# Optimization experiments

Hardware: AMD Instinct MI355X
Metric: run time of the kernel (lower is better)

## Reference

```python
import jax, jax.numpy as jnp
import numpy as np

N_NODES = 50000
N_EDGES = 800000
IN_DIM = 512
OUT_DIM = 512


def setup_inputs() -> dict:
    key = jax.random.key(0)
    ks = jax.random.split(key, 8)
    x = jax.random.normal(ks[0], (N_NODES, IN_DIM), dtype=jnp.float32)
    edge_index = jax.random.randint(ks[1], (2, N_EDGES), 0, N_NODES, dtype=jnp.int64)
    s = 1.0 / np.sqrt(IN_DIM)
    # SAGEConv params: lin_l (applied to aggregated neighbors, with bias),
    # lin_r (applied to root/self features, no bias). Two convs: loc and scale.
    Wl1 = jax.random.uniform(ks[2], (OUT_DIM, IN_DIM), jnp.float32, -s, s)
    bl1 = jnp.zeros((OUT_DIM,), jnp.float32)
    Wr1 = jax.random.uniform(ks[3], (OUT_DIM, IN_DIM), jnp.float32, -s, s)
    Wl2 = jax.random.uniform(ks[4], (OUT_DIM, IN_DIM), jnp.float32, -s, s)
    bl2 = jnp.zeros((OUT_DIM,), jnp.float32)
    Wr2 = jax.random.uniform(ks[5], (OUT_DIM, IN_DIM), jnp.float32, -s, s)
    return {"x": x, "edge_index": edge_index,
            "Wl1": Wl1, "bl1": bl1, "Wr1": Wr1,
            "Wl2": Wl2, "bl2": bl2, "Wr2": Wr2}


def _sage_conv(x, agg, Wl, bl, Wr):
    # lin_l(sum-aggregated neighbors) + lin_r(x)
    return agg @ Wl.T + bl + x @ Wr.T


def reference(x, edge_index, Wl1, bl1, Wr1, Wl2, bl2, Wr2):
    src, dst = edge_index[0], edge_index[1]
    # sum aggregation of source features into destination nodes: [N, in_dim]
    agg = jax.ops.segment_sum(x[src], dst, num_segments=N_NODES)
    loc = _sage_conv(x, agg, Wl1, bl1, Wr1)
    loc = jnp.clip(loc, -100.0, 100.0)
    scale = jax.nn.softplus(_sage_conv(x, agg, Wl2, bl2, Wr2)) + 0.001
    scale = jnp.minimum(scale, 100.0)
    return (loc, scale)
```

## Files before the change

kernel.cpp:

```cpp
#include <hip/hip_runtime.h>
#include <stdint.h>

#define N_NODES 50000
#define N_EDGES 800000
#define IN_DIM 512
#define OUT_DIM 512
#define KDIM 1024
#define NDIM 1024

typedef __bf16 bf16x8 __attribute__((ext_vector_type(8)));
typedef float f32x4 __attribute__((ext_vector_type(4)));

__device__ __forceinline__ unsigned short f2bf(float f) {
    union { float f; unsigned u; } c; c.f = f;
    unsigned u = c.u;
    u += 0x7fffu + ((u >> 16) & 1u);
    return (unsigned short)(u >> 16);
}
__device__ __forceinline__ float bf2f(unsigned short h) {
    union { unsigned u; float f; } c; c.u = ((unsigned)h) << 16;
    return c.f;
}

__global__ void xconv_kernel(const float* __restrict__ x, unsigned short* __restrict__ xb) {
    int i = blockIdx.x * blockDim.x + threadIdx.x;
    const int n4 = N_NODES * IN_DIM / 4;
    if (i < n4) {
        float4 v = ((const float4*)x)[i];
        ushort4 o;
        o.x = f2bf(v.x); o.y = f2bf(v.y); o.z = f2bf(v.z); o.w = f2bf(v.w);
        ((ushort4*)xb)[i] = o;
    }
}

__global__ void count_kernel(const int* __restrict__ ei, int* __restrict__ counts) {
    int i = blockIdx.x * blockDim.x + threadIdx.x;
    if (i < N_EDGES) {
        int dst = ei[N_EDGES + i];
        dst = min(max(dst, 0), N_NODES - 1);
        atomicAdd(&counts[dst], 1);
    }
}

__global__ __launch_bounds__(1024) void scan_local_kernel(
    const int* __restrict__ cnt, int* __restrict__ offs,
    int* __restrict__ bsums, int n) {
    __shared__ int warp_sums[16];
    int tid = threadIdx.x;
    int lane = tid & 63;
    int w = tid >> 6;
    int i = blockIdx.x * 1024 + tid;
    int v = (i < n) ? cnt[i] : 0;
    int s = v;
    #pragma unroll
    for (int d = 1; d < 64; d <<= 1) {
        int t = __shfl_up(s, d, 64);
        if (lane >= d) s += t;
    }
    if (lane == 63) warp_sums[w] = s;
    __syncthreads();
    if (w == 0) {
        int ws = (lane < 16) ? warp_sums[lane] : 0;
        #pragma unroll
        for (int d = 1; d < 16; d <<= 1) {
            int t = __shfl_up(ws, d, 64);
            if (lane >= d) ws += t;
        }
        if (lane < 16) warp_sums[lane] = ws;
    }
    __syncthreads();
    int base = (w > 0 ? warp_sums[w - 1] : 0);
    if (i < n) offs[i] = base + s - v;
    if (tid == 1023) bsums[blockIdx.x] = base + s;
}

__global__ void scan_bsums_kernel(int* __restrict__ bsums, int nb) {
    int lane = threadIdx.x & 63;
    int v = (lane < nb) ? bsums[lane] : 0;
    int s = v;
    #pragma unroll
    for (int d = 1; d < 64; d <<= 1) {
        int t = __shfl_up(s, d, 64);
        if (lane >= d) s += t;
    }
    if (lane < nb) bsums[lane] = s - v;
}

__global__ __launch_bounds__(1024) void scan_apply_kernel(
    int* __restrict__ offs, int* __restrict__ cursor,
    const int* __restrict__ bsums, const int* __restrict__ cnt, int n) {
    int i = blockIdx.x * 1024 + threadIdx.x;
    if (i < n) {
        int o = offs[i] + bsums[blockIdx.x];
        offs[i] = o;
        cursor[i] = o;
        if (i == n - 1) offs[n] = o + cnt[i];
    }
}

__global__ void fill_kernel(const int* __restrict__ ei, int* __restrict__ cursor,
                            int* __restrict__ bucket) {
    int i = blockIdx.x * blockDim.x + threadIdx.x;
    if (i < N_EDGES) {
        int src = ei[i];
        int dst = ei[N_EDGES + i];
        src = min(max(src, 0), N_NODES - 1);
        dst = min(max(dst, 0), N_NODES - 1);
        int pos = atomicAdd(&cursor[dst], 1);
        bucket[pos] = src;
    }
}

__global__ __launch_bounds__(256) void aggregate_kernel(
    const unsigned short* __restrict__ xb, const int* __restrict__ offs,
    const int* __restrict__ bucket, unsigned short* __restrict__ aggb) {
    int wid = threadIdx.x >> 6;
    int lane = threadIdx.x & 63;
    int n = blockIdx.x * 4 + wid;
    if (n >= N_NODES) return;
    int beg = offs[n], end = offs[n + 1];
    float a0[8] = {}, a1[8] = {};
    int e = beg;
    for (; e + 4 <= end; e += 4) {
        int s0 = bucket[e + 0];
        int s1 = bucket[e + 1];
        int s2 = bucket[e + 2];
        int s3 = bucket[e + 3];
        uint4 v0 = *(const uint4*)(xb + (size_t)s0 * IN_DIM + lane * 8);
        uint4 v1 = *(const uint4*)(xb + (size_t)s1 * IN_DIM + lane * 8);
        uint4 v2 = *(const uint4*)(xb + (size_t)s2 * IN_DIM + lane * 8);
        uint4 v3 = *(const uint4*)(xb + (size_t)s3 * IN_DIM + lane * 8);
        a0[0] += bf2f((unsigned short)(v0.x & 0xffffu)); a0[1] += bf2f((unsigned short)(v0.x >> 16));
        a0[2] += bf2f((unsigned short)(v0.y & 0xffffu)); a0[3] += bf2f((unsigned short)(v0.y >> 16));
        a0[4] += bf2f((unsigned short)(v0.z & 0xffffu)); a0[5] += bf2f((unsigned short)(v0.z >> 16));
        a0[6] += bf2f((unsigned short)(v0.w & 0xffffu)); a0[7] += bf2f((unsigned short)(v0.w >> 16));
        a1[0] += bf2f((unsigned short)(v1.x & 0xffffu)); a1[1] += bf2f((unsigned short)(v1.x >> 16));
        a1[2] += bf2f((unsigned short)(v1.y & 0xffffu)); a1[3] += bf2f((unsigned short)(v1.y >> 16));
        a1[4] += bf2f((unsigned short)(v1.z & 0xffffu)); a1[5] += bf2f((unsigned short)(v1.z >> 16));
        a1[6] += bf2f((unsigned short)(v1.w & 0xffffu)); a1[7] += bf2f((unsigned short)(v1.w >> 16));
        a0[0] += bf2f((unsigned short)(v2.x & 0xffffu)); a0[1] += bf2f((unsigned short)(v2.x >> 16));
        a0[2] += bf2f((unsigned short)(v2.y & 0xffffu)); a0[3] += bf2f((unsigned short)(v2.y >> 16));
        a0[4] += bf2f((unsigned short)(v2.z & 0xffffu)); a0[5] += bf2f((unsigned short)(v2.z >> 16));
        a0[6] += bf2f((unsigned short)(v2.w & 0xffffu)); a0[7] += bf2f((unsigned short)(v2.w >> 16));
        a1[0] += bf2f((unsigned short)(v3.x & 0xffffu)); a1[1] += bf2f((unsigned short)(v3.x >> 16));
        a1[2] += bf2f((unsigned short)(v3.y & 0xffffu)); a1[3] += bf2f((unsigned short)(v3.y >> 16));
        a1[4] += bf2f((unsigned short)(v3.z & 0xffffu)); a1[5] += bf2f((unsigned short)(v3.z >> 16));
        a1[6] += bf2f((unsigned short)(v3.w & 0xffffu)); a1[7] += bf2f((unsigned short)(v3.w >> 16));
    }
    for (; e < end; ++e) {
        int s = bucket[e];
        uint4 v = *(const uint4*)(xb + (size_t)s * IN_DIM + lane * 8);
        a0[0] += bf2f((unsigned short)(v.x & 0xffffu)); a0[1] += bf2f((unsigned short)(v.x >> 16));
        a0[2] += bf2f((unsigned short)(v.y & 0xffffu)); a0[3] += bf2f((unsigned short)(v.y >> 16));
        a0[4] += bf2f((unsigned short)(v.z & 0xffffu)); a0[5] += bf2f((unsigned short)(v.z >> 16));
        a0[6] += bf2f((unsigned short)(v.w & 0xffffu)); a0[7] += bf2f((unsigned short)(v.w >> 16));
    }
    uint4 o;
    o.x = (unsigned)f2bf(a0[0] + a1[0]) | ((unsigned)f2bf(a0[1] + a1[1]) << 16);
    o.y = (unsigned)f2bf(a0[2] + a1[2]) | ((unsigned)f2bf(a0[3] + a1[3]) << 16);
    o.z = (unsigned)f2bf(a0[4] + a1[4]) | ((unsigned)f2bf(a0[5] + a1[5]) << 16);
    o.w = (unsigned)f2bf(a0[6] + a1[6]) | ((unsigned)f2bf(a0[7] + a1[7]) << 16);
    *(uint4*)(aggb + (size_t)n * IN_DIM + lane * 8) = o;
}

__global__ void wconv_kernel(const float* __restrict__ Wl1, const float* __restrict__ Wr1,
                             const float* __restrict__ Wl2, const float* __restrict__ Wr2,
                             unsigned short* __restrict__ Wb) {
    int i = blockIdx.x * blockDim.x + threadIdx.x;
    if (i < NDIM * KDIM) {
        int n = i >> 10, k = i & 1023;
        const float* src;
        if (n < 512) src = (k < 512) ? Wl1 : Wr1;
        else         src = (k < 512) ? Wl2 : Wr2;
        int nn = n & 511, kk = k & 511;
        Wb[i] = f2bf(src[nn * 512 + kk]);
    }
}

#define BM 128
#define BN 128
#define BK 64
#define NT_TILES (NDIM / BN)
#define MT_TILES ((N_NODES + BM - 1) / BM)
#define NWG (NT_TILES * MT_TILES)

__device__ __forceinline__ void async_copy16(const void* g, void* lds) {
    __builtin_amdgcn_global_load_lds((const __attribute__((address_space(1))) void*)g,
                                     (__attribute__((address_space(3))) void*)lds, 16, 0, 0);
}

__global__ __launch_bounds__(256, 2) void gemm_kernel(
    const unsigned short* __restrict__ aggb,
    const unsigned short* __restrict__ xb,
    const unsigned short* __restrict__ Wb,
    const float* __restrict__ bl1, const float* __restrict__ bl2,
    float* __restrict__ out) {
    constexpr int M = N_NODES;
    __shared__ unsigned short sA[BM * BK];
    __shared__ unsigned short sB[BN * BK];

    int bid = blockIdx.x;
    int logical = (bid & 7) * (NWG / 8) + (bid >> 3);
    int nt = logical & (NT_TILES - 1);
    int mt = logical >> 3;
    int n0 = nt * BN;
    int m0 = mt * BM;

    int tid = threadIdx.x;
    int lane = tid & 63;
    int w = tid >> 6;
    int wm = (w >> 1) * 64, wn = (w & 1) * 64;

    f32x4 acc[4][4] = {};

    int fr = lane & 15, q = lane >> 4;
    int sl0 = ((q ^ (fr & 7)) << 3);
    int sl1 = (((q + 4) ^ (fr & 7)) << 3);

    for (int k0 = 0; k0 < KDIM; k0 += BK) {
        const unsigned short* Asrc;
        int ak;
        if (k0 < 512) { Asrc = aggb; ak = k0; } else { Asrc = xb; ak = k0 - 512; }
        #pragma unroll
        for (int iss = 0; iss < 4; ++iss) {
            int C = iss * 256 + tid;
            int r = C >> 3, p = C & 7;
            int gr = m0 + r; if (gr >= M) gr = M - 1;
            const unsigned short* g = Asrc + (size_t)gr * 512 + ak + ((p ^ (r & 7)) << 3);
            async_copy16(g, sA + (size_t)(iss * 256 + w * 64) * 8);
        }
        #pragma unroll
        for (int iss = 0; iss < 4; ++iss) {
            int C = iss * 256 + tid;
            int r = C >> 3, p = C & 7;
            const unsigned short* g = Wb + (size_t)(n0 + r) * KDIM + k0 + ((p ^ (r & 7)) << 3);
            async_copy16(g, sB + (size_t)(iss * 256 + w * 64) * 8);
        }
        __syncthreads();

        #pragma unroll
        for (int ksub = 0; ksub < 2; ++ksub) {
            int sl = ksub ? sl1 : sl0;
            bf16x8 af[4], bfg[4];
            #pragma unroll
            for (int i = 0; i < 4; ++i)
                af[i] = *(const bf16x8*)(sA + (wm + i * 16 + fr) * BK + sl);
            #pragma unroll
            for (int j = 0; j < 4; ++j)
                bfg[j] = *(const bf16x8*)(sB + (wn + j * 16 + fr) * BK + sl);
            #pragma unroll
            for (int i = 0; i < 4; ++i)
                #pragma unroll
                for (int j = 0; j < 4; ++j)
                    acc[i][j] = __builtin_amdgcn_mfma_f32_16x16x32_bf16(af[i], bfg[j], acc[i][j], 0, 0, 0);
        }
        __syncthreads();
    }

    bool is_scale = (n0 >= 512);
    const float* bias = is_scale ? bl2 : bl1;
    float* obase = out + (is_scale ? (size_t)N_NODES * OUT_DIM : 0);
    int ncol0 = is_scale ? (n0 - 512) : n0;
    int rq = lane >> 4;
    #pragma unroll
    for (int i = 0; i < 4; ++i) {
        #pragma unroll
        for (int j = 0; j < 4; ++j) {
            int colg = ncol0 + wn + j * 16 + fr;
            float b = bias[colg];
            #pragma unroll
            for (int r = 0; r < 4; ++r) {
                int rowg = m0 + wm + i * 16 + rq * 4 + r;
                if (rowg < M) {
                    float v = acc[i][j][r] + b;
                    float res;
                    if (is_scale) {
                        float sp = fmaxf(v, 0.f) + __logf(1.f + __expf(-fabsf(v)));
                        res = fminf(sp + 0.001f, 100.f);
                    } else {
                        res = fminf(fmaxf(v, -100.f), 100.f);
                    }
                    __builtin_nontemporal_store(res, &obase[(size_t)rowg * OUT_DIM + colg]);
                }
            }
        }
    }
}

extern "C" void kernel_launch(void* const* d_in, const int* in_sizes, int n_in,
                              void* d_out, int out_size, void* d_ws, size_t ws_size,
                              hipStream_t stream) {
    const float* x       = (const float*)d_in[0];
    const int* ei        = (const int*)d_in[1];
    const float* Wl1     = (const float*)d_in[2];
    const float* bl1     = (const float*)d_in[3];
    const float* Wr1     = (const float*)d_in[4];
    const float* Wl2     = (const float*)d_in[5];
    const float* bl2     = (const float*)d_in[6];
    const float* Wr2     = (const float*)d_in[7];
    float* out = (float*)d_out;

    char* ws = (char*)d_ws;
    size_t off = 0;
    auto alloc = [&](size_t bytes) -> void* {
        void* p = ws + off;
        off = (off + bytes + 255) & ~(size_t)255;
        return p;
    };
    unsigned short* xb    = (unsigned short*)alloc((size_t)N_NODES * IN_DIM * 2);
    unsigned short* aggb  = (unsigned short*)alloc((size_t)N_NODES * IN_DIM * 2);
    unsigned short* Wb    = (unsigned short*)alloc((size_t)NDIM * KDIM * 2);
    int* counts           = (int*)alloc((size_t)(N_NODES + 1) * 4);
    int* offs             = (int*)alloc((size_t)(N_NODES + 1) * 4);
    int* cursor           = (int*)alloc((size_t)N_NODES * 4);
    int* bucket           = (int*)alloc((size_t)N_EDGES * 4);
    int* bsums            = (int*)alloc(64 * 4);

    hipMemsetAsync(counts, 0, (size_t)(N_NODES + 1) * 4, stream);

    const int nb = (N_NODES + 1023) / 1024;

    xconv_kernel<<<(N_NODES * IN_DIM / 4 + 255) / 256, 256, 0, stream>>>(x, xb);
    count_kernel<<<(N_EDGES + 255) / 256, 256, 0, stream>>>(ei, counts);
    scan_local_kernel<<<nb, 1024, 0, stream>>>(counts, offs, bsums, N_NODES);
    scan_bsums_kernel<<<1, 64, 0, stream>>>(bsums, nb);
    scan_apply_kernel<<<nb, 1024, 0, stream>>>(offs, cursor, bsums, counts, N_NODES);
    fill_kernel<<<(N_EDGES + 255) / 256, 256, 0, stream>>>(ei, cursor, bucket);
    aggregate_kernel<<<(N_NODES + 3) / 4, 256, 0, stream>>>(xb, offs, bucket, aggb);
    wconv_kernel<<<(NDIM * KDIM + 255) / 256, 256, 0, stream>>>(Wl1, Wr1, Wl2, Wr2, Wb);

    gemm_kernel<<<NWG, 256, 0, stream>>>(aggb, xb, Wb, bl1, bl2, out);
}
```

Measured before the change: 600.0 us.

## Enlarge GEMM tiles to 256x256 with double-buffered staged pipeline and deeper gather unroll

The GEMM moves from 128x128 tiles with 256 threads and a single LDS buffer to 256x256 tiles with 512 threads. It uses a double-buffered 128KB LDS layout, and async global-to-LDS staging of the next k-tile is interleaved between four MFMA quadrants, with explicit vmcnt waits, raw s_barrier and s_setprio around MFMA bursts. The aim is to hide load latency behind compute and to raise data reuse per block. Separately, the aggregation gather loop is unrolled from 4 to 8 edges to put more loads in flight. The cost is high register pressure from 32 accumulators per lane, lower occupancy from the large LDS footprint, and fewer, larger blocks, which can leave more tail imbalance.

```diff
diff --git a/kernel.cpp b/kernel.cpp
--- a/kernel.cpp
+++ b/kernel.cpp
@@ -121,31 +121,21 @@
     int beg = offs[n], end = offs[n + 1];
     float a0[8] = {}, a1[8] = {};
     int e = beg;
-    for (; e + 4 <= end; e += 4) {
-        int s0 = bucket[e + 0];
-        int s1 = bucket[e + 1];
-        int s2 = bucket[e + 2];
-        int s3 = bucket[e + 3];
-        uint4 v0 = *(const uint4*)(xb + (size_t)s0 * IN_DIM + lane * 8);
-        uint4 v1 = *(const uint4*)(xb + (size_t)s1 * IN_DIM + lane * 8);
-        uint4 v2 = *(const uint4*)(xb + (size_t)s2 * IN_DIM + lane * 8);
-        uint4 v3 = *(const uint4*)(xb + (size_t)s3 * IN_DIM + lane * 8);
-        a0[0] += bf2f((unsigned short)(v0.x & 0xffffu)); a0[1] += bf2f((unsigned short)(v0.x >> 16));
-        a0[2] += bf2f((unsigned short)(v0.y & 0xffffu)); a0[3] += bf2f((unsigned short)(v0.y >> 16));
-        a0[4] += bf2f((unsigned short)(v0.z & 0xffffu)); a0[5] += bf2f((unsigned short)(v0.z >> 16));
-        a0[6] += bf2f((unsigned short)(v0.w & 0xffffu)); a0[7] += bf2f((unsigned short)(v0.w >> 16));
-        a1[0] += bf2f((unsigned short)(v1.x & 0xffffu)); a1[1] += bf2f((unsigned short)(v1.x >> 16));
-        a1[2] += bf2f((unsigned short)(v1.y & 0xffffu)); a1[3] += bf2f((unsigned short)(v1.y >> 16));
-        a1[4] += bf2f((unsigned short)(v1.z & 0xffffu)); a1[5] += bf2f((unsigned short)(v1.z >> 16));
-        a1[6] += bf2f((unsigned short)(v1.w & 0xffffu)); a1[7] += bf2f((unsigned short)(v1.w >> 16));
-        a0[0] += bf2f((unsigned short)(v2.x & 0xffffu)); a0[1] += bf2f((unsigned short)(v2.x >> 16));
-        a0[2] += bf2f((unsigned short)(v2.y & 0xffffu)); a0[3] += bf2f((unsigned short)(v2.y >> 16));
-        a0[4] += bf2f((unsigned short)(v2.z & 0xffffu)); a0[5] += bf2f((unsigned short)(v2.z >> 16));
-        a0[6] += bf2f((unsigned short)(v2.w & 0xffffu)); a0[7] += bf2f((unsigned short)(v2.w >> 16));
-        a1[0] += bf2f((unsigned short)(v3.x & 0xffffu)); a1[1] += bf2f((unsigned short)(v3.x >> 16));
-        a1[2] += bf2f((unsigned short)(v3.y & 0xffffu)); a1[3] += bf2f((unsigned short)(v3.y >> 16));
-        a1[4] += bf2f((unsigned short)(v3.z & 0xffffu)); a1[5] += bf2f((unsigned short)(v3.z >> 16));
-        a1[6] += bf2f((unsigned short)(v3.w & 0xffffu)); a1[7] += bf2f((unsigned short)(v3.w >> 16));
+    for (; e + 8 <= end; e += 8) {
+        int idx[8];
+        #pragma unroll
+        for (int u = 0; u < 8; ++u) idx[u] = bucket[e + u];
+        uint4 v[8];
+        #pragma unroll
+        for (int u = 0; u < 8; ++u) v[u] = *(const uint4*)(xb + (size_t)idx[u] * IN_DIM + lane * 8);
+        #pragma unroll
+        for (int u = 0; u < 8; ++u) {
+            float* a = (u & 1) ? a1 : a0;
+            a[0] += bf2f((unsigned short)(v[u].x & 0xffffu)); a[1] += bf2f((unsigned short)(v[u].x >> 16));
+            a[2] += bf2f((unsigned short)(v[u].y & 0xffffu)); a[3] += bf2f((unsigned short)(v[u].y >> 16));
+            a[4] += bf2f((unsigned short)(v[u].z & 0xffffu)); a[5] += bf2f((unsigned short)(v[u].z >> 16));
+            a[6] += bf2f((unsigned short)(v[u].w & 0xffffu)); a[7] += bf2f((unsigned short)(v[u].w >> 16));
+        }
     }
     for (; e < end; ++e) {
         int s = bucket[e];
@@ -177,84 +167,132 @@
     }
 }
 
-#define BM 128
-#define BN 128
+#define BM 256
+#define BN 256
 #define BK 64
-#define NT_TILES (NDIM / BN)
-#define MT_TILES ((N_NODES + BM - 1) / BM)
-#define NWG (NT_TILES * MT_TILES)
+#define NTT (NDIM / BN)
+#define MTT ((N_NODES + BM - 1) / BM)
+#define NWG (NTT * MTT)
+#define NKT (KDIM / BK)
 
 __device__ __forceinline__ void async_copy16(const void* g, void* lds) {
     __builtin_amdgcn_global_load_lds((const __attribute__((address_space(1))) void*)g,
                                      (__attribute__((address_space(3))) void*)lds, 16, 0, 0);
 }
-
-__global__ __launch_bounds__(256, 2) void gemm_kernel(
+#define BAR() asm volatile("s_barrier" ::: "memory")
+
+__device__ __forceinline__ void stage_half(
+    const unsigned short* __restrict__ src, int row0, int stride, int rowmax,
+    int kcol0, unsigned short* ldsb, int tid) {
+    #pragma unroll
+    for (int iss = 0; iss < 2; ++iss) {
+        int C = iss * 512 + tid;
+        int lr = C >> 3, p = C & 7;
+        int gr = row0 + lr; if (gr > rowmax) gr = rowmax;
+        const unsigned short* g = src + (size_t)gr * stride + kcol0 + ((p ^ (lr & 7)) << 3);
+        async_copy16(g, ldsb + (size_t)(iss * 512 + (tid & ~63)) * 8);
+    }
+}
+
+__global__ __launch_bounds__(512, 2) void gemm_kernel(
     const unsigned short* __restrict__ aggb,
     const unsigned short* __restrict__ xb,
     const unsigned short* __restrict__ Wb,
     const float* __restrict__ bl1, const float* __restrict__ bl2,
     float* __restrict__ out) {
     constexpr int M = N_NODES;
-    __shared__ unsigned short sA[BM * BK];
-    __shared__ unsigned short sB[BN * BK];
+    __shared__ unsigned short lds[65536];
 
     int bid = blockIdx.x;
     int logical = (bid & 7) * (NWG / 8) + (bid >> 3);
-    int nt = logical & (NT_TILES - 1);
-    int mt = logical >> 3;
+    int nt = logical & (NTT - 1);
+    int mt = logical >> 2;
     int n0 = nt * BN;
     int m0 = mt * BM;
 
     int tid = threadIdx.x;
     int lane = tid & 63;
     int w = tid >> 6;
-    int wm = (w >> 1) * 64, wn = (w & 1) * 64;
-
-    f32x4 acc[4][4] = {};
+    int wr = w >> 2;
+    int wc = w & 3;
 
     int fr = lane & 15, q = lane >> 4;
     int sl0 = ((q ^ (fr & 7)) << 3);
     int sl1 = (((q + 4) ^ (fr & 7)) << 3);
 
-    for (int k0 = 0; k0 < KDIM; k0 += BK) {
-        const unsigned short* Asrc;
-        int ak;
-        if (k0 < 512) { Asrc = aggb; ak = k0; } else { Asrc = xb; ak = k0 - 512; }
-        #pragma unroll
-        for (int iss = 0; iss < 4; ++iss) {
-            int C = iss * 256 + tid;
-            int r = C >> 3, p = C & 7;
-            int gr = m0 + r; if (gr >= M) gr = M - 1;
-            const unsigned short* g = Asrc + (size_t)gr * 512 + ak + ((p ^ (r & 7)) << 3);
-            async_copy16(g, sA + (size_t)(iss * 256 + w * 64) * 8);
-        }
-        #pragma unroll
-        for (int iss = 0; iss < 4; ++iss) {
-            int C = iss * 256 + tid;
-            int r = C >> 3, p = C & 7;
-            const unsigned short* g = Wb + (size_t)(n0 + r) * KDIM + k0 + ((p ^ (r & 7)) << 3);
-            async_copy16(g, sB + (size_t)(iss * 256 + w * 64) * 8);
-        }
-        __syncthreads();
-
-        #pragma unroll
-        for (int ksub = 0; ksub < 2; ++ksub) {
-            int sl = ksub ? sl1 : sl0;
-            bf16x8 af[4], bfg[4];
-            #pragma unroll
-            for (int i = 0; i < 4; ++i)
-                af[i] = *(const bf16x8*)(sA + (wm + i * 16 + fr) * BK + sl);
-            #pragma unroll
-            for (int j = 0; j < 4; ++j)
-                bfg[j] = *(const bf16x8*)(sB + (wn + j * 16 + fr) * BK + sl);
-            #pragma unroll
-            for (int i = 0; i < 4; ++i)
-                #pragma unroll
-                for (int j = 0; j < 4; ++j)
-                    acc[i][j] = __builtin_amdgcn_mfma_f32_16x16x32_bf16(af[i], bfg[j], acc[i][j], 0, 0, 0);
-        }
-        __syncthreads();
+    f32x4 acc[8][4] = {};
+    bf16x8 aF[4][2], bF[4][2];
+
+    auto STAGE_A = [&](int t, int h) {
+        if (t >= NKT) return;
+        int kk = t * 64;
+        const unsigned short* s = (kk < 512) ? aggb : xb;
+        stage_half(s, m0 + h * 128, 512, M - 1, kk & 511,
+                   &lds[(size_t)(t & 1) * 16384 + h * 8192], tid);
+    };
+    auto STAGE_B = [&](int t, int h) {
+        if (t >= NKT) return;
+        stage_half(Wb, n0 + h * 128, 1024, NDIM - 1, t * 64,
+                   &lds[32768 + (size_t)(t & 1) * 16384 + h * 8192], tid);
+    };
+    auto LOAD_A = [&](int t, int ra) {
+        const unsigned short* base = &lds[(size_t)(t & 1) * 16384 + wr * 8192];
+        #pragma unroll
+        for (int i = 0; i < 4; ++i) {
+            int lr = ra * 64 + i * 16 + fr;
+            aF[i][0] = *(const bf16x8*)(base + lr * 64 + sl0);
+            aF[i][1] = *(const bf16x8*)(base + lr * 64 + sl1);
+        }
+    };
+    auto LOAD_B = [&](int t, int cb) {
+        const unsigned short* base = &lds[32768 + (size_t)(t & 1) * 16384 + (wc >> 1) * 8192];
+        #pragma unroll
+        for (int jj = 0; jj < 2; ++jj) {
+            int lr = (wc & 1) * 64 + (cb * 2 + jj) * 16 + fr;
+            bF[cb * 2 + jj][0] = *(const bf16x8*)(base + lr * 64 + sl0);
+            bF[cb * 2 + jj][1] = *(const bf16x8*)(base + lr * 64 + sl1);
+        }
+    };
+    #define MFMA_Q(RA, CB)                                                          \
+        __builtin_amdgcn_s_setprio(1);                                              \
+        _Pragma("unroll")                                                           \
+        for (int i = 0; i < 4; ++i)                                                 \
+            _Pragma("unroll")                                                       \
+            for (int jj = 0; jj < 2; ++jj)                                          \
+                _Pragma("unroll")                                                   \
+                for (int ks = 0; ks < 2; ++ks)                                      \
+                    acc[(RA) * 4 + i][(CB) * 2 + jj] =                              \
+                        __builtin_amdgcn_mfma_f32_16x16x32_bf16(                    \
+                            aF[i][ks], bF[(CB) * 2 + jj][ks],                       \
+                            acc[(RA) * 4 + i][(CB) * 2 + jj], 0, 0, 0);             \
+        __builtin_amdgcn_s_setprio(0);
+
+    STAGE_A(0, 0); STAGE_A(0, 1); STAGE_B(0, 0); STAGE_B(0, 1); STAGE_A(1, 0);
+    asm volatile("s_waitcnt vmcnt(2)" ::: "memory");
+    BAR();
+
+    for (int t = 0; t < NKT; ++t) {
+        LOAD_A(t, 0); LOAD_B(t, 0);
+        STAGE_A(t + 1, 1);
+        BAR();
+        MFMA_Q(0, 0);
+        BAR();
+        LOAD_B(t, 1);
+        STAGE_B(t + 1, 0);
+        BAR();
+        MFMA_Q(0, 1);
+        BAR();
+        LOAD_A(t, 1);
+        STAGE_B(t + 1, 1);
+        BAR();
+        MFMA_Q(1, 0);
+        BAR();
+        STAGE_A(t + 2, 0);
+        if (t <= NKT - 3)      { asm volatile("s_waitcnt vmcnt(2)" ::: "memory"); }
+        else if (t == NKT - 2) { asm volatile("s_waitcnt vmcnt(0)" ::: "memory"); }
+        BAR();
+        MFMA_Q(1, 1);
+        BAR();
     }
 
     bool is_scale = (n0 >= 512);
@@ -263,16 +301,16 @@
     int ncol0 = is_scale ? (n0 - 512) : n0;
     int rq = lane >> 4;
     #pragma unroll
-    for (int i = 0; i < 4; ++i) {
-        #pragma unroll
-        for (int j = 0; j < 4; ++j) {
-            int colg = ncol0 + wn + j * 16 + fr;
-            float b = bias[colg];
+    for (int j = 0; j < 4; ++j) {
+        int colg = ncol0 + wc * 64 + j * 16 + fr;
+        float b = bias[colg];
+        #pragma unroll
+        for (int ia = 0; ia < 8; ++ia) {
             #pragma unroll
             for (int r = 0; r < 4; ++r) {
-                int rowg = m0 + wm + i * 16 + rq * 4 + r;
+                int rowg = m0 + wr * 128 + ia * 16 + rq * 4 + r;
                 if (rowg < M) {
-                    float v = acc[i][j][r] + b;
+                    float v = acc[ia][j][r] + b;
                     float res;
                     if (is_scale) {
                         float sp = fmaxf(v, 0.f) + __logf(1.f + __expf(-fabsf(v)));
@@ -285,6 +323,7 @@
             }
         }
     }
+    #undef MFMA_Q
 }
 
 extern "C" void kernel_launch(void* const* d_in, const int* in_sizes, int n_in,
@@ -329,5 +368,5 @@
     aggregate_kernel<<<(N_NODES + 3) / 4, 256, 0, stream>>>(xb, offs, bucket, aggb);
     wconv_kernel<<<(NDIM * KDIM + 255) / 256, 256, 0, stream>>>(Wl1, Wr1, Wl2, Wr2, Wb);
 
-    gemm_kernel<<<NWG, 256, 0, stream>>>(aggb, xb, Wb, bl1, bl2, out);
-}
+    gemm_kernel<<<NWG, 512, 0, stream>>>(aggb, xb, Wb, bl1, bl2, out);
+}
```

After: 667.8 us. 1.11x slower.
